# Optimization experiments

Hardware: AMD Instinct MI355X
Metric: run time of the kernel (lower is better)

The kernel has to match this reference:

```python
import jax, jax.numpy as jnp
import numpy as np

N_NODES = 100000
N_EDGES = 1600000
N_GRAPHS = 512
D_IN = 128
D_H = 128
D_GF = 32
N_LAYERS = 3


def setup_inputs() -> dict:
    key = jax.random.key(0)
    ks = jax.random.split(key, 16)
    s = 1.0 / np.sqrt(D_H)
    inp = {
        "x": jax.random.normal(ks[0], (N_NODES, D_IN), dtype=jnp.float32),
        "edge_index": jax.random.randint(ks[1], (2, N_EDGES), 0, N_NODES, dtype=jnp.int64),
        "batch_idx": jnp.sort(jax.random.randint(ks[2], (N_NODES,), 0, N_GRAPHS, dtype=jnp.int64)),
        "graph_feat": jax.random.normal(ks[3], (N_GRAPHS, D_GF), dtype=jnp.float32),
        # input projection
        "W_in": jax.random.normal(ks[4], (D_IN, D_H), dtype=jnp.float32) * s,
        "b_in": jnp.zeros((D_H,), dtype=jnp.float32),
        # SAGEConv params (stacked over layers): lin_l (neighbor, with bias), lin_r (self, no bias)
        "Wl": jax.random.normal(ks[5], (N_LAYERS, D_H, D_H), dtype=jnp.float32) * s,
        "bl": jnp.zeros((N_LAYERS, D_H), dtype=jnp.float32),
        "Wr": jax.random.normal(ks[6], (N_LAYERS, D_H, D_H), dtype=jnp.float32) * s,
        # output MLP head
        "W1": jax.random.normal(ks[7], (2 * D_H + D_GF, D_H), dtype=jnp.float32) * (1.0 / np.sqrt(2 * D_H + D_GF)),
        "b1": jnp.zeros((D_H,), dtype=jnp.float32),
        "W2": jax.random.normal(ks[8], (D_H, D_H), dtype=jnp.float32) * s,
        "b2": jnp.zeros((D_H,), dtype=jnp.float32),
    }
    return inp


def _sage_conv(h, src, dst, Wl, bl, Wr):
    # mean aggregation of neighbor (source) features at target nodes
    ones = jnp.ones((src.shape[0],), dtype=h.dtype)
    deg = jax.ops.segment_sum(ones, dst, num_segments=N_NODES)
    agg = jax.ops.segment_sum(h[src], dst, num_segments=N_NODES)
    agg = agg / jnp.maximum(deg, 1.0)[:, None]
    return agg @ Wl + bl + h @ Wr


def reference(x, edge_index, batch_idx, graph_feat, W_in, b_in, Wl, bl, Wr, W1, b1, W2, b2):
    src, dst = edge_index[0], edge_index[1]
    h = jax.nn.relu(x @ W_in + b_in)
    for l in range(N_LAYERS):
        h = jax.nn.relu(_sage_conv(h, src, dst, Wl[l], bl[l], Wr[l]))
        # dropout is identity in eval mode
    # global mean / max pool over graphs
    ones = jnp.ones((N_NODES,), dtype=h.dtype)
    cnt = jax.ops.segment_sum(ones, batch_idx, num_segments=N_GRAPHS)
    mean_p = jax.ops.segment_sum(h, batch_idx, num_segments=N_GRAPHS) / jnp.maximum(cnt, 1.0)[:, None]
    max_p = jax.ops.segment_max(h, batch_idx, num_segments=N_GRAPHS)
    pooled = jnp.concatenate([mean_p, max_p], axis=-1)
    gf = graph_feat.reshape(pooled.shape[0], -1)
    z = jnp.concatenate([pooled, gf], axis=-1)
    z = jax.nn.relu(z @ W1 + b1)
    return jax.nn.relu(z @ W2 + b2)
```

## Files before the change

kernel.cpp:

```cpp
#include <hip/hip_runtime.h>

#define N_NODES  100000
#define N_EDGES  1600000
#define N_GRAPHS 512
#define D_H      128
#define N_LAYERS 3

typedef __attribute__((ext_vector_type(8))) short bf16x8;
typedef __attribute__((ext_vector_type(4))) float f32x4;

__device__ __forceinline__ unsigned short f2bf(float f) {
    unsigned int u = __float_as_uint(f);
    u += 0x7fffu + ((u >> 16) & 1u);
    return (unsigned short)(u >> 16);
}
__device__ __forceinline__ float bf2f(unsigned short h) {
    return __uint_as_float(((unsigned int)h) << 16);
}
__device__ __forceinline__ float bflo(unsigned v) { return __uint_as_float(v << 16); }
__device__ __forceinline__ float bfhi(unsigned v) { return __uint_as_float(v & 0xffff0000u); }

#define BM  128
#define BKP 72

template <int MODE>
__global__ __launch_bounds__(256) void gemm_mfma(
    const float* __restrict__ Af, const unsigned short* A0,
    const unsigned short* A1, const unsigned short* __restrict__ BT,
    const float* __restrict__ bias, unsigned short* out, int M)
{
    constexpr int Ktot = (MODE == 0) ? 128 : 256;
    __shared__ unsigned short As[BM][BKP];
    __shared__ unsigned short Bs[128][BKP];

    const int t    = threadIdx.x;
    const int wave = t >> 6, lane = t & 63;
    const int wr   = wave >> 1, wc = wave & 1;
    const int row0 = blockIdx.x * BM;

    f32x4 acc[4][4];
#pragma unroll
    for (int m = 0; m < 4; m++)
#pragma unroll
        for (int n = 0; n < 4; n++) acc[m][n] = (f32x4)0.f;

    for (int s = 0; s < (Ktot >> 6); s++) {
        const int kb = s * 64;
        __syncthreads();
        if (MODE == 0) {
#pragma unroll
            for (int it = 0; it < 4; it++) {
                const int idx = t + it * 256;
                const int r = idx >> 3, c8 = (idx & 7) * 8;
                uint4 o = make_uint4(0, 0, 0, 0);
                if (row0 + r < M) {
                    const float* p = &Af[(size_t)(row0 + r) * D_H + kb + c8];
                    const float4 v0 = *(const float4*)p;
                    const float4 v1 = *(const float4*)(p + 4);
                    o.x = (unsigned)f2bf(v0.x) | ((unsigned)f2bf(v0.y) << 16);
                    o.y = (unsigned)f2bf(v0.z) | ((unsigned)f2bf(v0.w) << 16);
                    o.z = (unsigned)f2bf(v1.x) | ((unsigned)f2bf(v1.y) << 16);
                    o.w = (unsigned)f2bf(v1.z) | ((unsigned)f2bf(v1.w) << 16);
                }
                *(uint4*)&As[r][c8] = o;
            }
        } else {
            const unsigned short* Asrc = (kb < 128) ? A0 : A1;
            const int ka = kb & 127;
#pragma unroll
            for (int it = 0; it < 4; it++) {
                const int idx = t + it * 256;
                const int r = idx >> 3, c8 = (idx & 7) * 8;
                uint4 v = make_uint4(0, 0, 0, 0);
                if (row0 + r < M)
                    v = *(const uint4*)&Asrc[(size_t)(row0 + r) * D_H + ka + c8];
                *(uint4*)&As[r][c8] = v;
            }
        }
#pragma unroll
        for (int it = 0; it < 4; it++) {
            const int idx = t + it * 256;
            const int n = idx >> 3, c8 = (idx & 7) * 8;
            *(uint4*)&Bs[n][c8] = *(const uint4*)&BT[(size_t)n * Ktot + kb + c8];
        }
        __syncthreads();

#pragma unroll
        for (int kk = 0; kk < 64; kk += 32) {
            const int koff = kk + (lane >> 4) * 8;
            bf16x8 af[4], bfr[4];
#pragma unroll
            for (int m = 0; m < 4; m++)
                af[m] = *(const bf16x8*)&As[wr * 64 + m * 16 + (lane & 15)][koff];
#pragma unroll
            for (int n = 0; n < 4; n++)
                bfr[n] = *(const bf16x8*)&Bs[wc * 64 + n * 16 + (lane & 15)][koff];
#pragma unroll
            for (int m = 0; m < 4; m++)
#pragma unroll
                for (int n = 0; n < 4; n++)
                    acc[m][n] = __builtin_amdgcn_mfma_f32_16x16x32_bf16(
                        af[m], bfr[n], acc[m][n], 0, 0, 0);
        }
    }

    float bv[4];
#pragma unroll
    for (int n = 0; n < 4; n++) bv[n] = bias[wc * 64 + n * 16 + (lane & 15)];

#pragma unroll
    for (int m = 0; m < 4; m++) {
#pragma unroll
        for (int j = 0; j < 4; j++) {
            const int row = row0 + wr * 64 + m * 16 + (lane >> 4) * 4 + j;
            if (row < M) {
#pragma unroll
                for (int n = 0; n < 4; n++) {
                    const int col = wc * 64 + n * 16 + (lane & 15);
                    out[(size_t)row * D_H + col] = f2bf(fmaxf(acc[m][n][j] + bv[n], 0.f));
                }
            }
        }
    }
}

__global__ __launch_bounds__(256) void prep_bt(
    const float* __restrict__ W_in, const float* __restrict__ Wl,
    const float* __restrict__ Wr, unsigned short* __restrict__ BTin,
    unsigned short* __restrict__ BTl)
{
    const int i = blockIdx.x * blockDim.x + threadIdx.x;
    if (i < 128 * 128) {
        const int n = i >> 7, k = i & 127;
        BTin[n * 128 + k] = f2bf(W_in[k * 128 + n]);
    } else if (i < 128 * 128 + N_LAYERS * 128 * 256) {
        const int j = i - 128 * 128;
        const int l = j >> 15, r = j & 32767;
        const int n = r >> 8, k = r & 255;
        const float v = (k < 128) ? Wl[(size_t)l * 16384 + k * 128 + n]
                                  : Wr[(size_t)l * 16384 + (k - 128) * 128 + n];
        BTl[(size_t)l * 32768 + n * 256 + k] = f2bf(v);
    }
}

#define NBUK 256
#define EPB  8192
#define NBLK ((N_EDGES + EPB - 1) / EPB)

__global__ __launch_bounds__(256) void csr_count(
    const int* __restrict__ dst, int* __restrict__ cntMat)
{
    __shared__ int cnt[NBUK];
    cnt[threadIdx.x] = 0;
    __syncthreads();
    const int e0 = blockIdx.x * EPB;
    const int e1 = min(e0 + EPB, N_EDGES);
    for (int e = e0 + threadIdx.x; e < e1; e += 256)
        atomicAdd(&cnt[dst[e] >> 9], 1);
    __syncthreads();
    cntMat[threadIdx.x * NBLK + blockIdx.x] = cnt[threadIdx.x];
}

__global__ __launch_bounds__(256) void csr_scan_bucket(
    const int* __restrict__ cntMat, int* __restrict__ basMat, int* __restrict__ btot)
{
    __shared__ int s[256];
    const int b = blockIdx.x, t = threadIdx.x;
    const int v = (t < NBLK) ? cntMat[b * NBLK + t] : 0;
    s[t] = v; __syncthreads();
    for (int st = 1; st < 256; st <<= 1) {
        const int u = (t >= st) ? s[t - st] : 0;
        __syncthreads();
        s[t] += u;
        __syncthreads();
    }
    if (t < NBLK) basMat[b * NBLK + t] = s[t] - v;
    if (t == 255) btot[b] = s[255];
}

__global__ __launch_bounds__(256) void csr_scan_top(
    const int* __restrict__ btot, int* __restrict__ bbase)
{
    __shared__ int s[NBUK];
    const int t = threadIdx.x;
    const int v = btot[t];
    s[t] = v; __syncthreads();
    for (int st = 1; st < 256; st <<= 1) {
        const int u = (t >= st) ? s[t - st] : 0;
        __syncthreads();
        s[t] += u;
        __syncthreads();
    }
    bbase[t] = s[t] - v;
}

__global__ __launch_bounds__(256) void csr_scatter(
    const int* __restrict__ src, const int* __restrict__ dst,
    const int* __restrict__ basMat, const int* __restrict__ bbase,
    int2* __restrict__ binned)
{
    __shared__ int cur[NBUK];
    cur[threadIdx.x] = bbase[threadIdx.x] + basMat[threadIdx.x * NBLK + blockIdx.x];
    __syncthreads();
    const int e0 = blockIdx.x * EPB;
    const int e1 = min(e0 + EPB, N_EDGES);
    for (int e = e0 + threadIdx.x; e < e1; e += 256) {
        const int d = dst[e];
        const int pos = atomicAdd(&cur[d >> 9], 1);
        binned[pos] = make_int2(src[e], d);
    }
}

__global__ __launch_bounds__(256) void csr_build(
    const int2* __restrict__ binned, const int* __restrict__ bbase,
    const int* __restrict__ btot, int* __restrict__ rp, int* __restrict__ deg,
    float* __restrict__ inv, int* __restrict__ csr)
{
    __shared__ int hist[512];
    __shared__ int psc[256];
    __shared__ int cur[512];
    const int b = blockIdx.x, t = threadIdx.x;
    const int base = bbase[b];
    const int cntE = btot[b];
    const int n0 = b << 9;

    hist[t] = 0; hist[t + 256] = 0;
    __syncthreads();
    for (int i = t; i < cntE; i += 256)
        atomicAdd(&hist[binned[base + i].y - n0], 1);
    __syncthreads();

    const int h0 = hist[2 * t], h1 = hist[2 * t + 1];
    const int own = h0 + h1;
    psc[t] = own; __syncthreads();
    for (int st = 1; st < 256; st <<= 1) {
        const int u = (t >= st) ? psc[t - st] : 0;
        __syncthreads();
        psc[t] += u;
        __syncthreads();
    }
    const int pairExcl = psc[t] - own;
    cur[2 * t]     = pairExcl;
    cur[2 * t + 1] = pairExcl + h0;
    const int node0 = n0 + 2 * t, node1 = n0 + 2 * t + 1;
    if (node0 < N_NODES) {
        rp[node0] = base + pairExcl; deg[node0] = h0;
        inv[node0] = 1.f / fmaxf((float)h0, 1.f);
    }
    if (node1 < N_NODES) {
        rp[node1] = base + pairExcl + h0; deg[node1] = h1;
        inv[node1] = 1.f / fmaxf((float)h1, 1.f);
    }
    __syncthreads();
    for (int i = t; i < cntE; i += 256) {
        const int2 r = binned[base + i];
        const int pos = atomicAdd(&cur[r.y - n0], 1);
        csr[base + pos] = r.x;
    }
}

__global__ __launch_bounds__(256) void gather_mean(
    const unsigned short* __restrict__ h, const int* __restrict__ csr,
    const int* __restrict__ rp, const int* __restrict__ deg,
    const float* __restrict__ inv, unsigned short* __restrict__ agg)
{
    const int wave   = (blockIdx.x * blockDim.x + threadIdx.x) >> 6;
    const int lane   = threadIdx.x & 63;
    const int grp    = lane >> 4;
    const int fl     = (lane & 15) * 8;
    const int nwaves = (gridDim.x * blockDim.x) >> 6;

    for (int n = wave; n < N_NODES; n += nwaves) {
        const int s0 = rp[n];
        const int s1 = s0 + deg[n];
        float a[8];
#pragma unroll
        for (int k = 0; k < 8; k++) a[k] = 0.f;

        for (int j = s0 + grp; j < s1; j += 4) {
            const int s = csr[j];
            const uint4 v = *(const uint4*)&h[(size_t)s * D_H + fl];
            a[0] += bflo(v.x); a[1] += bfhi(v.x);
            a[2] += bflo(v.y); a[3] += bfhi(v.y);
            a[4] += bflo(v.z); a[5] += bfhi(v.z);
            a[6] += bflo(v.w); a[7] += bfhi(v.w);
        }
#pragma unroll
        for (int k = 0; k < 8; k++) a[k] += __shfl_xor(a[k], 16, 64);
#pragma unroll
        for (int k = 0; k < 8; k++) a[k] += __shfl_xor(a[k], 32, 64);

        if (grp == 0) {
            const float sc = inv[n];
            uint4 o;
            o.x = (unsigned)f2bf(a[0] * sc) | ((unsigned)f2bf(a[1] * sc) << 16);
            o.y = (unsigned)f2bf(a[2] * sc) | ((unsigned)f2bf(a[3] * sc) << 16);
            o.z = (unsigned)f2bf(a[4] * sc) | ((unsigned)f2bf(a[5] * sc) << 16);
            o.w = (unsigned)f2bf(a[6] * sc) | ((unsigned)f2bf(a[7] * sc) << 16);
            *(uint4*)&agg[(size_t)n * D_H + fl] = o;
        }
    }
}

__global__ __launch_bounds__(256) void pool_graph(
    const unsigned short* __restrict__ h, const int* __restrict__ batch,
    float* __restrict__ meanb, float* __restrict__ maxb)
{
    __shared__ int bounds[2];
    __shared__ float2 ssum[256];
    __shared__ float2 smax[256];
    const int g = blockIdx.x, t = threadIdx.x;
    if (t < 2) {
        const int v = g + t;
        int lo = 0, hi = N_NODES;
        while (lo < hi) { const int m = (lo + hi) >> 1; if (batch[m] < v) lo = m + 1; else hi = m; }
        bounds[t] = lo;
    }
    __syncthreads();
    const int n0 = bounds[0], n1 = bounds[1];
    const int f2 = t & 63;
    const int sub = t >> 6;

    float sx = 0.f, sy = 0.f, mx = 0.f, my = 0.f;
    for (int n = n0 + sub; n < n1; n += 4) {
        const unsigned v = *(const unsigned*)&h[(size_t)n * D_H + f2 * 2];
        const float x = bflo(v), y = bfhi(v);
        sx += x; sy += y;
        mx = fmaxf(mx, x); my = fmaxf(my, y);
    }
    ssum[t] = make_float2(sx, sy);
    smax[t] = make_float2(mx, my);
    __syncthreads();
    if (sub == 0) {
        const float2 s0 = ssum[t], s1 = ssum[t + 64], s2 = ssum[t + 128], s3 = ssum[t + 192];
        const float2 m0 = smax[t], m1 = smax[t + 64], m2 = smax[t + 128], m3 = smax[t + 192];
        const float ic = 1.f / fmaxf((float)(n1 - n0), 1.f);
        meanb[g * D_H + f2 * 2]     = (s0.x + s1.x + s2.x + s3.x) * ic;
        meanb[g * D_H + f2 * 2 + 1] = (s0.y + s1.y + s2.y + s3.y) * ic;
        maxb[g * D_H + f2 * 2]      = fmaxf(fmaxf(m0.x, m1.x), fmaxf(m2.x, m3.x));
        maxb[g * D_H + f2 * 2 + 1]  = fmaxf(fmaxf(m0.y, m1.y), fmaxf(m2.y, m3.y));
    }
}

__global__ __launch_bounds__(128) void mlp_kernel(
    const float* __restrict__ meanb, const float* __restrict__ maxb,
    const float* __restrict__ gf,
    const float* __restrict__ W1, const float* __restrict__ b1,
    const float* __restrict__ W2, const float* __restrict__ b2,
    float* __restrict__ out)
{
    __shared__ float z[2 * D_H + 32];
    __shared__ float z1[D_H];
    const int g = blockIdx.x, t = threadIdx.x;
    z[t]       = meanb[g * D_H + t];
    z[D_H + t] = maxb[g * D_H + t];
    if (t < 32) z[2 * D_H + t] = gf[g * 32 + t];
    __syncthreads();
    float a = b1[t];
    for (int k = 0; k < 2 * D_H + 32; k++) a += z[k] * W1[k * D_H + t];
    a = fmaxf(a, 0.f);
    z1[t] = a;
    __syncthreads();
    float o = b2[t];
    for (int k = 0; k < D_H; k++) o += z1[k] * W2[k * D_H + t];
    out[g * D_H + t] = fmaxf(o, 0.f);
}

extern "C" void kernel_launch(void* const* d_in, const int* in_sizes, int n_in,
                              void* d_out, int out_size, void* d_ws, size_t ws_size,
                              hipStream_t stream)
{
    const float* x     = (const float*)d_in[0];
    const int*   ei    = (const int*)d_in[1];
    const int*   batch = (const int*)d_in[2];
    const float* gf    = (const float*)d_in[3];
    const float* W_in  = (const float*)d_in[4];
    const float* b_in  = (const float*)d_in[5];
    const float* Wl    = (const float*)d_in[6];
    const float* bl    = (const float*)d_in[7];
    const float* Wr    = (const float*)d_in[8];
    const float* W1    = (const float*)d_in[9];
    const float* b1    = (const float*)d_in[10];
    const float* W2    = (const float*)d_in[11];
    const float* b2    = (const float*)d_in[12];
    float* out = (float*)d_out;

    const int* srcI = ei;
    const int* dstI = ei + N_EDGES;

    char* ws = (char*)d_ws;
    size_t off = 0;
    auto alloc = [&](size_t bytes) {
        char* p = ws + off;
        off += (bytes + 511) / 512 * 512;
        return p;
    };
    const size_t hB16 = (size_t)N_NODES * D_H * sizeof(unsigned short);
    unsigned short* bufA = (unsigned short*)alloc(hB16);
    unsigned short* bufB = (unsigned short*)alloc(hB16);
    unsigned short* BTin = (unsigned short*)alloc(128 * 128 * sizeof(unsigned short));
    unsigned short* BTl  = (unsigned short*)alloc((size_t)N_LAYERS * 128 * 256 * sizeof(unsigned short));
    int*   degI   = (int*)alloc(N_NODES * sizeof(int));
    float* inv    = (float*)alloc(N_NODES * sizeof(float));
    int*   rp     = (int*)alloc(N_NODES * sizeof(int));
    int*   csr    = (int*)alloc((size_t)N_EDGES * sizeof(int));
    int2*  binned = (int2*)alloc((size_t)N_EDGES * sizeof(int2));
    int*   cntMat = (int*)alloc((size_t)NBUK * NBLK * sizeof(int));
    int*   basMat = (int*)alloc((size_t)NBUK * NBLK * sizeof(int));
    int*   btot   = (int*)alloc(NBUK * sizeof(int));
    int*   bbase  = (int*)alloc(NBUK * sizeof(int));
    float* meanb  = (float*)alloc(N_GRAPHS * D_H * sizeof(float));
    float* maxb   = (float*)alloc(N_GRAPHS * D_H * sizeof(float));

    csr_count<<<NBLK, 256, 0, stream>>>(dstI, cntMat);
    csr_scan_bucket<<<NBUK, 256, 0, stream>>>(cntMat, basMat, btot);
    csr_scan_top<<<1, 256, 0, stream>>>(btot, bbase);
    csr_scatter<<<NBLK, 256, 0, stream>>>(srcI, dstI, basMat, bbase, binned);
    csr_build<<<NBUK, 256, 0, stream>>>(binned, bbase, btot, rp, degI, inv, csr);

    prep_bt<<<(128 * 128 + N_LAYERS * 128 * 256 + 255) / 256, 256, 0, stream>>>(
        W_in, Wl, Wr, BTin, BTl);

    const int gblocks = (N_NODES + BM - 1) / BM;
    gemm_mfma<0><<<gblocks, 256, 0, stream>>>(x, nullptr, nullptr, BTin, b_in, bufA, N_NODES);

    unsigned short* h   = bufA;
    unsigned short* agg = bufB;
    for (int l = 0; l < N_LAYERS; l++) {
        gather_mean<<<2048, 256, 0, stream>>>(h, csr, rp, degI, inv, agg);
        gemm_mfma<1><<<gblocks, 256, 0, stream>>>(nullptr, agg, h, BTl + (size_t)l * 32768,
                                                  bl + (size_t)l * D_H, agg, N_NODES);
        unsigned short* tmp = h; h = agg; agg = tmp;
    }

    pool_graph<<<N_GRAPHS, 256, 0, stream>>>(h, batch, meanb, maxb);
    mlp_kernel<<<N_GRAPHS, 128, 0, stream>>>(meanb, maxb, gf, W1, b1, W2, b2, out);
}
```

Before: 386.4 us.

## Fuse neighbor mean-gather into per-layer SAGE GEMM via shared-memory aggregate tile

Each layer now runs one kernel. Every block first gathers and mean-aggregates neighbor features for its 128 rows into an LDS tile, then runs the MFMA GEMM over [agg | h] with the combined weights. This removes the separate gather kernel launch and the global round-trip of the bf16 agg buffer. In exchange, the gather runs with only 782 blocks of 4 waves each, and each wave handles 32 rows serially, so latency hiding for the random gathers may drop. The larger LDS footprint also lowers occupancy.

```diff
diff --git a/kernel.cpp b/kernel.cpp
--- a/kernel.cpp
+++ b/kernel.cpp
@@ -22,14 +22,12 @@
 
 #define BM  128
 #define BKP 72
-
-template <int MODE>
-__global__ __launch_bounds__(256) void gemm_mfma(
-    const float* __restrict__ Af, const unsigned short* A0,
-    const unsigned short* A1, const unsigned short* __restrict__ BT,
+#define AGP 132
+
+__global__ __launch_bounds__(256) void gemm_in(
+    const float* __restrict__ Af, const unsigned short* __restrict__ BT,
     const float* __restrict__ bias, unsigned short* out, int M)
 {
-    constexpr int Ktot = (MODE == 0) ? 128 : 256;
     __shared__ unsigned short As[BM][BKP];
     __shared__ unsigned short Bs[128][BKP];
 
@@ -44,28 +42,133 @@
 #pragma unroll
         for (int n = 0; n < 4; n++) acc[m][n] = (f32x4)0.f;
 
-    for (int s = 0; s < (Ktot >> 6); s++) {
+    for (int s = 0; s < 2; s++) {
         const int kb = s * 64;
         __syncthreads();
-        if (MODE == 0) {
-#pragma unroll
-            for (int it = 0; it < 4; it++) {
-                const int idx = t + it * 256;
-                const int r = idx >> 3, c8 = (idx & 7) * 8;
-                uint4 o = make_uint4(0, 0, 0, 0);
-                if (row0 + r < M) {
-                    const float* p = &Af[(size_t)(row0 + r) * D_H + kb + c8];
-                    const float4 v0 = *(const float4*)p;
-                    const float4 v1 = *(const float4*)(p + 4);
-                    o.x = (unsigned)f2bf(v0.x) | ((unsigned)f2bf(v0.y) << 16);
-                    o.y = (unsigned)f2bf(v0.z) | ((unsigned)f2bf(v0.w) << 16);
-                    o.z = (unsigned)f2bf(v1.x) | ((unsigned)f2bf(v1.y) << 16);
-                    o.w = (unsigned)f2bf(v1.z) | ((unsigned)f2bf(v1.w) << 16);
+#pragma unroll
+        for (int it = 0; it < 4; it++) {
+            const int idx = t + it * 256;
+            const int r = idx >> 3, c8 = (idx & 7) * 8;
+            uint4 o = make_uint4(0, 0, 0, 0);
+            if (row0 + r < M) {
+                const float* p = &Af[(size_t)(row0 + r) * D_H + kb + c8];
+                const float4 v0 = *(const float4*)p;
+                const float4 v1 = *(const float4*)(p + 4);
+                o.x = (unsigned)f2bf(v0.x) | ((unsigned)f2bf(v0.y) << 16);
+                o.y = (unsigned)f2bf(v0.z) | ((unsigned)f2bf(v0.w) << 16);
+                o.z = (unsigned)f2bf(v1.x) | ((unsigned)f2bf(v1.y) << 16);
+                o.w = (unsigned)f2bf(v1.z) | ((unsigned)f2bf(v1.w) << 16);
+            }
+            *(uint4*)&As[r][c8] = o;
+        }
+#pragma unroll
+        for (int it = 0; it < 4; it++) {
+            const int idx = t + it * 256;
+            const int n = idx >> 3, c8 = (idx & 7) * 8;
+            *(uint4*)&Bs[n][c8] = *(const uint4*)&BT[(size_t)n * 128 + kb + c8];
+        }
+        __syncthreads();
+
+#pragma unroll
+        for (int kk = 0; kk < 64; kk += 32) {
+            const int koff = kk + (lane >> 4) * 8;
+            bf16x8 af[4], bfr[4];
+#pragma unroll
+            for (int m = 0; m < 4; m++)
+                af[m] = *(const bf16x8*)&As[wr * 64 + m * 16 + (lane & 15)][koff];
+#pragma unroll
+            for (int n = 0; n < 4; n++)
+                bfr[n] = *(const bf16x8*)&Bs[wc * 64 + n * 16 + (lane & 15)][koff];
+#pragma unroll
+            for (int m = 0; m < 4; m++)
+#pragma unroll
+                for (int n = 0; n < 4; n++)
+                    acc[m][n] = __builtin_amdgcn_mfma_f32_16x16x32_bf16(
+                        af[m], bfr[n], acc[m][n], 0, 0, 0);
+        }
+    }
+
+    float bv[4];
+#pragma unroll
+    for (int n = 0; n < 4; n++) bv[n] = bias[wc * 64 + n * 16 + (lane & 15)];
+#pragma unroll
+    for (int m = 0; m < 4; m++) {
+#pragma unroll
+        for (int j = 0; j < 4; j++) {
+            const int row = row0 + wr * 64 + m * 16 + (lane >> 4) * 4 + j;
+            if (row < M) {
+#pragma unroll
+                for (int n = 0; n < 4; n++) {
+                    const int col = wc * 64 + n * 16 + (lane & 15);
+                    out[(size_t)row * D_H + col] = f2bf(fmaxf(acc[m][n][j] + bv[n], 0.f));
                 }
-                *(uint4*)&As[r][c8] = o;
-            }
-        } else {
-            const unsigned short* Asrc = (kb < 128) ? A0 : A1;
+            }
+        }
+    }
+}
+
+__global__ __launch_bounds__(256) void layer_fused(
+    const unsigned short* __restrict__ h, const int* __restrict__ csr,
+    const int* __restrict__ rp, const int* __restrict__ deg,
+    const float* __restrict__ inv, const unsigned short* __restrict__ BT,
+    const float* __restrict__ bias, unsigned short* __restrict__ out, int M)
+{
+    __shared__ unsigned short Agg[BM][AGP];
+    __shared__ unsigned short As[BM][BKP];
+    __shared__ unsigned short Bs[128][BKP];
+
+    const int t    = threadIdx.x;
+    const int wave = t >> 6, lane = t & 63;
+    const int wr   = wave >> 1, wc = wave & 1;
+    const int grp  = lane >> 4;
+    const int fl   = (lane & 15) * 8;
+    const int row0 = blockIdx.x * BM;
+
+    f32x4 acc[4][4];
+#pragma unroll
+    for (int m = 0; m < 4; m++)
+#pragma unroll
+        for (int n = 0; n < 4; n++) acc[m][n] = (f32x4)0.f;
+
+    for (int i = 0; i < 32; i++) {
+        const int r = wave * 32 + i;
+        const int n = row0 + r;
+        if (n < M) {
+            const int s0 = rp[n];
+            const int s1 = s0 + deg[n];
+            float a[8];
+#pragma unroll
+            for (int k = 0; k < 8; k++) a[k] = 0.f;
+            for (int j = s0 + grp; j < s1; j += 4) {
+                const int s = csr[j];
+                const uint4 v = *(const uint4*)&h[(size_t)s * D_H + fl];
+                a[0] += bflo(v.x); a[1] += bfhi(v.x);
+                a[2] += bflo(v.y); a[3] += bfhi(v.y);
+                a[4] += bflo(v.z); a[5] += bfhi(v.z);
+                a[6] += bflo(v.w); a[7] += bfhi(v.w);
+            }
+#pragma unroll
+            for (int k = 0; k < 8; k++) a[k] += __shfl_xor(a[k], 16, 64);
+#pragma unroll
+            for (int k = 0; k < 8; k++) a[k] += __shfl_xor(a[k], 32, 64);
+            if (grp == 0) {
+                const float sc = inv[n];
+                uint4 o;
+                o.x = (unsigned)f2bf(a[0] * sc) | ((unsigned)f2bf(a[1] * sc) << 16);
+                o.y = (unsigned)f2bf(a[2] * sc) | ((unsigned)f2bf(a[3] * sc) << 16);
+                o.z = (unsigned)f2bf(a[4] * sc) | ((unsigned)f2bf(a[5] * sc) << 16);
+                o.w = (unsigned)f2bf(a[6] * sc) | ((unsigned)f2bf(a[7] * sc) << 16);
+                *(uint4*)&Agg[r][fl] = o;
+            }
+        } else if (grp == 0) {
+            *(uint4*)&Agg[r][fl] = make_uint4(0, 0, 0, 0);
+        }
+    }
+
+    for (int s = 0; s < 4; s++) {
+        const int kb = s * 64;
+        __syncthreads();
+        if (s >= 2) {
             const int ka = kb & 127;
 #pragma unroll
             for (int it = 0; it < 4; it++) {
@@ -73,7 +176,7 @@
                 const int r = idx >> 3, c8 = (idx & 7) * 8;
                 uint4 v = make_uint4(0, 0, 0, 0);
                 if (row0 + r < M)
-                    v = *(const uint4*)&Asrc[(size_t)(row0 + r) * D_H + ka + c8];
+                    v = *(const uint4*)&h[(size_t)(row0 + r) * D_H + ka + c8];
                 *(uint4*)&As[r][c8] = v;
             }
         }
@@ -81,7 +184,7 @@
         for (int it = 0; it < 4; it++) {
             const int idx = t + it * 256;
             const int n = idx >> 3, c8 = (idx & 7) * 8;
-            *(uint4*)&Bs[n][c8] = *(const uint4*)&BT[(size_t)n * Ktot + kb + c8];
+            *(uint4*)&Bs[n][c8] = *(const uint4*)&BT[(size_t)n * 256 + kb + c8];
         }
         __syncthreads();
 
@@ -89,9 +192,15 @@
         for (int kk = 0; kk < 64; kk += 32) {
             const int koff = kk + (lane >> 4) * 8;
             bf16x8 af[4], bfr[4];
-#pragma unroll
-            for (int m = 0; m < 4; m++)
-                af[m] = *(const bf16x8*)&As[wr * 64 + m * 16 + (lane & 15)][koff];
+            if (s < 2) {
+#pragma unroll
+                for (int m = 0; m < 4; m++)
+                    af[m] = *(const bf16x8*)&Agg[wr * 64 + m * 16 + (lane & 15)][kb + koff];
+            } else {
+#pragma unroll
+                for (int m = 0; m < 4; m++)
+                    af[m] = *(const bf16x8*)&As[wr * 64 + m * 16 + (lane & 15)][koff];
+            }
 #pragma unroll
             for (int n = 0; n < 4; n++)
                 bfr[n] = *(const bf16x8*)&Bs[wc * 64 + n * 16 + (lane & 15)][koff];
@@ -107,7 +216,6 @@
     float bv[4];
 #pragma unroll
     for (int n = 0; n < 4; n++) bv[n] = bias[wc * 64 + n * 16 + (lane & 15)];
-
 #pragma unroll
     for (int m = 0; m < 4; m++) {
 #pragma unroll
@@ -256,49 +364,6 @@
         const int2 r = binned[base + i];
         const int pos = atomicAdd(&cur[r.y - n0], 1);
         csr[base + pos] = r.x;
-    }
-}
-
-__global__ __launch_bounds__(256) void gather_mean(
-    const unsigned short* __restrict__ h, const int* __restrict__ csr,
-    const int* __restrict__ rp, const int* __restrict__ deg,
-    const float* __restrict__ inv, unsigned short* __restrict__ agg)
-{
-    const int wave   = (blockIdx.x * blockDim.x + threadIdx.x) >> 6;
-    const int lane   = threadIdx.x & 63;
-    const int grp    = lane >> 4;
-    const int fl     = (lane & 15) * 8;
-    const int nwaves = (gridDim.x * blockDim.x) >> 6;
-
-    for (int n = wave; n < N_NODES; n += nwaves) {
-        const int s0 = rp[n];
-        const int s1 = s0 + deg[n];
-        float a[8];
-#pragma unroll
-        for (int k = 0; k < 8; k++) a[k] = 0.f;
-
-        for (int j = s0 + grp; j < s1; j += 4) {
-            const int s = csr[j];
-            const uint4 v = *(const uint4*)&h[(size_t)s * D_H + fl];
-            a[0] += bflo(v.x); a[1] += bfhi(v.x);
-            a[2] += bflo(v.y); a[3] += bfhi(v.y);
-            a[4] += bflo(v.z); a[5] += bfhi(v.z);
-            a[6] += bflo(v.w); a[7] += bfhi(v.w);
-        }
-#pragma unroll
-        for (int k = 0; k < 8; k++) a[k] += __shfl_xor(a[k], 16, 64);
-#pragma unroll
-        for (int k = 0; k < 8; k++) a[k] += __shfl_xor(a[k], 32, 64);
-
-        if (grp == 0) {
-            const float sc = inv[n];
-            uint4 o;
-            o.x = (unsigned)f2bf(a[0] * sc) | ((unsigned)f2bf(a[1] * sc) << 16);
-            o.y = (unsigned)f2bf(a[2] * sc) | ((unsigned)f2bf(a[3] * sc) << 16);
-            o.z = (unsigned)f2bf(a[4] * sc) | ((unsigned)f2bf(a[5] * sc) << 16);
-            o.w = (unsigned)f2bf(a[6] * sc) | ((unsigned)f2bf(a[7] * sc) << 16);
-            *(uint4*)&agg[(size_t)n * D_H + fl] = o;
-        }
     }
 }
 
@@ -422,15 +487,15 @@
         W_in, Wl, Wr, BTin, BTl);
 
     const int gblocks = (N_NODES + BM - 1) / BM;
-    gemm_mfma<0><<<gblocks, 256, 0, stream>>>(x, nullptr, nullptr, BTin, b_in, bufA, N_NODES);
-
-    unsigned short* h   = bufA;
-    unsigned short* agg = bufB;
+    gemm_in<<<gblocks, 256, 0, stream>>>(x, BTin, b_in, bufA, N_NODES);
+
+    unsigned short* h  = bufA;
+    unsigned short* hn = bufB;
     for (int l = 0; l < N_LAYERS; l++) {
-        gather_mean<<<2048, 256, 0, stream>>>(h, csr, rp, degI, inv, agg);
-        gemm_mfma<1><<<gblocks, 256, 0, stream>>>(nullptr, agg, h, BTl + (size_t)l * 32768,
-                                                  bl + (size_t)l * D_H, agg, N_NODES);
-        unsigned short* tmp = h; h = agg; agg = tmp;
+        layer_fused<<<gblocks, 256, 0, stream>>>(h, csr, rp, degI, inv,
+                                                 BTl + (size_t)l * 32768,
+                                                 bl + (size_t)l * D_H, hn, N_NODES);
+        unsigned short* tmp = h; h = hn; hn = tmp;
     }
 
     pool_graph<<<N_GRAPHS, 256, 0, stream>>>(h, batch, meanb, maxb);
```

Result: slower. 867.0 us (+124.4%).
